# Performance work log

Measured on AMD Instinct MI355X. Metric: run time of the kernel, lower is better.

Reference implementation:

```python
import jax, jax.numpy as jnp
import numpy as np

N = 50000
D = 128
E = 800000
L = 3


def setup_inputs() -> dict:
    key = jax.random.key(0)
    ks = jax.random.split(key, 6)
    z = jax.random.normal(ks[0], (N, D), dtype=jnp.float32)
    edge_index = jax.random.randint(ks[1], (2, E), 0, N, dtype=jnp.int64)
    s1 = 1.0 / np.sqrt(2 * D)
    s2 = 1.0 / np.sqrt(D)
    # per-layer MLP params, stacked over layers: y = x @ W + b (W stored input-major)
    W1 = jax.random.uniform(ks[2], (L, 2 * D, D), jnp.float32, -s1, s1)
    b1 = jax.random.uniform(ks[3], (L, D), jnp.float32, -s1, s1)
    W2 = jax.random.uniform(ks[4], (L, D, D), jnp.float32, -s2, s2)
    b2 = jax.random.uniform(ks[5], (L, D), jnp.float32, -s2, s2)
    return {"z": z, "edge_index": edge_index, "W1": W1, "b1": b1, "W2": W2, "b2": b2}


def _edgeconv(h, src, dst, W1, b1, W2, b2):
    # message: mlp(cat[x_i, x_j]) per edge; x_i = target (dst), x_j = source (src)
    tmp = jnp.concatenate([h[dst], h[src]], axis=1)           # [E, 2D]
    m = jax.nn.relu(tmp @ W1 + b1) @ W2 + b2                  # [E, D]
    agg = jax.ops.segment_max(m, dst, num_segments=N)          # [N, D], -inf for empty
    return jnp.where(jnp.isfinite(agg), agg, 0.0)


def reference(z, edge_index, W1, b1, W2, b2):
    src = edge_index[0]
    dst = edge_index[1]
    h = z
    for l in range(L - 1):
        h = jax.nn.relu(_edgeconv(h, src, dst, W1[l], b1[l], W2[l], b2[l]))
    h = _edgeconv(h, src, dst, W1[L - 1], b1[L - 1], W2[L - 1], b2[L - 1])
    return h
```

## Files before the change

kernel.cpp:

```cpp
#include <hip/hip_runtime.h>

#define DH 128
#define NLAYER 3
typedef unsigned short ushort_t;
typedef __attribute__((ext_vector_type(8))) short bf16x8;
typedef __attribute__((ext_vector_type(4))) float f32x4;

__device__ __forceinline__ ushort_t f2bf(float a) {
    unsigned u = __float_as_uint(a);
    return (ushort_t)((u + 0x7fffu + ((u >> 16) & 1u)) >> 16);
}
__device__ __forceinline__ float bf2f(ushort_t h) {
    return __uint_as_float(((unsigned)h) << 16);
}
__device__ __forceinline__ unsigned cvtpk(float a, float b) {
    unsigned r;
    asm("v_cvt_pk_bf16_f32 %0, %1, %2" : "=v"(r) : "v"(a), "v"(b));
    return r;
}

__device__ __forceinline__ unsigned enc_f(float f) {
    unsigned u = __float_as_uint(f);
    return (u & 0x80000000u) ? ~u : (u | 0x80000000u);
}
__device__ __forceinline__ float dec_f(unsigned u) {
    unsigned b = (u & 0x80000000u) ? (u ^ 0x80000000u) : ~u;
    return __uint_as_float(b);
}
#define ENC_NEG_INF 0x007FFFFFu

__global__ void fill_u(unsigned* __restrict__ p, int n, unsigned v) {
    int i = blockIdx.x * blockDim.x + threadIdx.x;
    int stride = gridDim.x * blockDim.x;
    for (; i < n; i += stride) p[i] = v;
}

__global__ void hist_kernel(const int* __restrict__ dst, unsigned* __restrict__ cnt, int E) {
    int e = blockIdx.x * blockDim.x + threadIdx.x;
    int stride = gridDim.x * blockDim.x;
    for (; e < E; e += stride) atomicAdd(&cnt[dst[e]], 1u);
}

__global__ __launch_bounds__(1024) void scan_local(const unsigned* __restrict__ cnt,
                                                   unsigned* __restrict__ off,
                                                   unsigned* __restrict__ bsum, int n) {
    __shared__ unsigned s[1024];
    const int t = threadIdx.x;
    int idx = blockIdx.x * 1024 + t;
    unsigned v = (idx < n) ? cnt[idx] : 0u;
    s[t] = v;
    __syncthreads();
    for (int d = 1; d < 1024; d <<= 1) {
        unsigned u = (t >= d) ? s[t - d] : 0u;
        __syncthreads();
        s[t] += u;
        __syncthreads();
    }
    if (idx < n) off[idx] = s[t] - v;
    if (t == 1023) bsum[blockIdx.x] = s[t];
}
__global__ void scan_base(unsigned* __restrict__ bsum, int nb) {
    __shared__ unsigned s[64];
    const int t = threadIdx.x;
    unsigned v = (t < nb) ? bsum[t] : 0u;
    s[t] = v;
    __syncthreads();
    for (int d = 1; d < 64; d <<= 1) {
        unsigned u = (t >= d) ? s[t - d] : 0u;
        __syncthreads();
        s[t] += u;
        __syncthreads();
    }
    if (t < nb) bsum[t] = s[t] - v;
}
__global__ void scan_add(unsigned* __restrict__ off, const unsigned* __restrict__ bsum,
                         unsigned* __restrict__ cnt, int n) {
    int i = blockIdx.x * blockDim.x + threadIdx.x;
    int stride = gridDim.x * blockDim.x;
    for (; i < n; i += stride) { off[i] += bsum[i >> 10]; cnt[i] = 0u; }
}

__global__ void scatter_kernel(const int* __restrict__ src, const int* __restrict__ dst,
                               const unsigned* __restrict__ off, unsigned* __restrict__ cur,
                               int* __restrict__ s_src, int* __restrict__ s_dst, int E) {
    int e = blockIdx.x * blockDim.x + threadIdx.x;
    int stride = gridDim.x * blockDim.x;
    for (; e < E; e += stride) {
        int d = dst[e];
        unsigned p = off[d] + atomicAdd(&cur[d], 1u);
        s_src[p] = src[e];
        s_dst[p] = d;
    }
}

__global__ void convert_w(const float* __restrict__ W1, const float* __restrict__ W2,
                          ushort_t* __restrict__ W1t_hi, ushort_t* __restrict__ W1t_lo,
                          ushort_t* __restrict__ W2t_hi, ushort_t* __restrict__ W2t_lo) {
    const int T1 = NLAYER * 256 * DH, T2 = NLAYER * DH * DH;
    int i = blockIdx.x * blockDim.x + threadIdx.x;
    int stride = gridDim.x * blockDim.x;
    for (; i < T1 + T2; i += stride) {
        if (i < T1) {
            int l = i >> 15, r = i & 32767, c = r >> 7, k = r & 127;
            float w = W1[(size_t)l * 32768 + (size_t)((c < 128) ? k : 128 + k) * DH + (c & 127)];
            ushort_t hi = f2bf(w);
            W1t_hi[i] = hi; W1t_lo[i] = f2bf(w - bf2f(hi));
        } else {
            int j = i - T1;
            int l = j >> 14, r = j & 16383, c = r >> 7, k = r & 127;
            float w = W2[(size_t)l * 16384 + (size_t)k * DH + c];
            ushort_t hi = f2bf(w);
            W2t_hi[j] = hi; W2t_lo[j] = f2bf(w - bf2f(hi));
        }
    }
}

__global__ void convert_h(const float* __restrict__ z, unsigned* __restrict__ hpk, int n) {
    int i = blockIdx.x * blockDim.x + threadIdx.x;
    int stride = gridDim.x * blockDim.x;
    for (; i < n; i += stride) {
        float a = z[i];
        ushort_t hi = f2bf(a);
        ushort_t lo = f2bf(a - bf2f(hi));
        hpk[i] = (unsigned)hi | ((unsigned)lo << 16);
    }
}

__global__ __launch_bounds__(256, 2) void node_gemm(
    const unsigned* __restrict__ hpk,
    const ushort_t* __restrict__ wthi, const ushort_t* __restrict__ wtlo,
    const float* __restrict__ bias, float* __restrict__ outA, float* __restrict__ outB,
    int N, int nrb) {
    __shared__ char smem[65536];
    char* Whi = smem;
    char* Wlo = smem + 32768;
    const int bb = blockIdx.x;
    const int half = (bb >= nrb) ? 1 : 0;
    const ushort_t* whi = wthi + (half ? (size_t)128 * DH : 0);
    const ushort_t* wlo = wtlo + (half ? (size_t)128 * DH : 0);
    float* outp = half ? outB : outA;
    const int t = threadIdx.x;
    const int w = t >> 6, l = t & 63;
    for (int cid = t; cid < 2048; cid += 256) {
        int c = cid >> 4, ch = cid & 15;
        uint4 vh = *(const uint4*)(whi + (size_t)cid * 8);
        uint4 vl = *(const uint4*)(wlo + (size_t)cid * 8);
        *(uint4*)(Whi + c * 256 + ((ch ^ (c & 15)) << 4)) = vh;
        *(uint4*)(Wlo + c * 256 + ((ch ^ (c & 15)) << 4)) = vl;
    }
    const int n0 = (bb - half * nrb) * 128;
    bf16x8 ahi[2][4], alo[2][4];
    #pragma unroll
    for (int rt = 0; rt < 2; ++rt) {
        int row = n0 + w * 32 + rt * 16 + (l & 15);
        if (row >= N) row = N - 1;
        const unsigned* ph = hpk + (size_t)row * DH + 8 * (l >> 4);
        #pragma unroll
        for (int ks = 0; ks < 4; ++ks) {
            uint4 p0 = *(const uint4*)(ph + ks * 32);
            uint4 p1 = *(const uint4*)(ph + ks * 32 + 4);
            bf16x8 hv, lv;
            hv[0] = (short)(p0.x & 0xffffu); lv[0] = (short)(p0.x >> 16);
            hv[1] = (short)(p0.y & 0xffffu); lv[1] = (short)(p0.y >> 16);
            hv[2] = (short)(p0.z & 0xffffu); lv[2] = (short)(p0.z >> 16);
            hv[3] = (short)(p0.w & 0xffffu); lv[3] = (short)(p0.w >> 16);
            hv[4] = (short)(p1.x & 0xffffu); lv[4] = (short)(p1.x >> 16);
            hv[5] = (short)(p1.y & 0xffffu); lv[5] = (short)(p1.y >> 16);
            hv[6] = (short)(p1.z & 0xffffu); lv[6] = (short)(p1.z >> 16);
            hv[7] = (short)(p1.w & 0xffffu); lv[7] = (short)(p1.w >> 16);
            ahi[rt][ks] = hv; alo[rt][ks] = lv;
        }
    }
    f32x4 acc[2][8];
    #pragma unroll
    for (int rt = 0; rt < 2; ++rt)
        #pragma unroll
        for (int ct = 0; ct < 8; ++ct) acc[rt][ct] = (f32x4){0.f, 0.f, 0.f, 0.f};
    __syncthreads();
    #pragma unroll
    for (int ct = 0; ct < 8; ++ct) {
        int colv = ct * 16 + (l & 15);
        #pragma unroll
        for (int ks = 0; ks < 4; ++ks) {
            int chb = ks * 4 + (l >> 4);
            int addr = colv * 256 + ((chb ^ (colv & 15)) << 4);
            bf16x8 bh = *(const bf16x8*)(Whi + addr);
            bf16x8 bl = *(const bf16x8*)(Wlo + addr);
            #pragma unroll
            for (int rt = 0; rt < 2; ++rt) {
                acc[rt][ct] = __builtin_amdgcn_mfma_f32_16x16x32_bf16(ahi[rt][ks], bh, acc[rt][ct], 0, 0, 0);
                acc[rt][ct] = __builtin_amdgcn_mfma_f32_16x16x32_bf16(ahi[rt][ks], bl, acc[rt][ct], 0, 0, 0);
                acc[rt][ct] = __builtin_amdgcn_mfma_f32_16x16x32_bf16(alo[rt][ks], bh, acc[rt][ct], 0, 0, 0);
            }
        }
    }
    #pragma unroll
    for (int ct = 0; ct < 8; ++ct) {
        int col = ct * 16 + (l & 15);
        float bv = half ? 0.0f : bias[col];
        #pragma unroll
        for (int rt = 0; rt < 2; ++rt)
            #pragma unroll
            for (int i = 0; i < 4; ++i) {
                int row = n0 + w * 32 + rt * 16 + (l >> 4) * 4 + i;
                if (row < N) outp[(size_t)row * DH + col] = acc[rt][ct][i] + bv;
            }
    }
}

__global__ __launch_bounds__(256, 2) void edge_mlp(
    const float* __restrict__ Afp, const float* __restrict__ Bfp,
    const int* __restrict__ src, const int* __restrict__ dst,
    const ushort_t* __restrict__ w2hi, const ushort_t* __restrict__ w2lo,
    unsigned* __restrict__ agg, int E) {
    __shared__ char smem[33280];
    int* sdst = (int*)(smem + 32768);
    float* R = (float*)smem;
    const int t = threadIdx.x;
    const int w = t >> 6, l = t & 63;
    const int e0 = blockIdx.x * 128;

    if (t < 128) sdst[t] = dst[e0 + t];
    #pragma unroll
    for (int i = 0; i < 4; ++i) {
        int cid = i * 256 + t;
        int cc = cid >> 4, ch = cid & 15;
        int sc = ch ^ (cc & 15);
        uint4 vh = *(const uint4*)(w2hi + (size_t)cc * DH + sc * 8);
        uint4 vl = *(const uint4*)(w2lo + (size_t)cc * DH + sc * 8);
        *(uint4*)(smem + cid * 16) = vh;
        *(uint4*)(smem + 16384 + cid * 16) = vl;
    }

    bf16x8 ahi[2][4], alo[2][4];
    #pragma unroll
    for (int rt = 0; rt < 2; ++rt) {
        int er = w * 32 + rt * 16 + (l & 15);
        int dn = dst[e0 + er], sn = src[e0 + er];
        const float* pa = Afp + (size_t)dn * DH + 8 * (l >> 4);
        const float* pb = Bfp + (size_t)sn * DH + 8 * (l >> 4);
        #pragma unroll
        for (int ks = 0; ks < 4; ++ks) {
            float4 a0 = *(const float4*)(pa + ks * 32);
            float4 a1 = *(const float4*)(pa + ks * 32 + 4);
            float4 b0 = *(const float4*)(pb + ks * 32);
            float4 b1 = *(const float4*)(pb + ks * 32 + 4);
            float v0 = fmaxf(a0.x + b0.x, 0.f), v1 = fmaxf(a0.y + b0.y, 0.f);
            float v2 = fmaxf(a0.z + b0.z, 0.f), v3 = fmaxf(a0.w + b0.w, 0.f);
            float v4 = fmaxf(a1.x + b1.x, 0.f), v5 = fmaxf(a1.y + b1.y, 0.f);
            float v6 = fmaxf(a1.z + b1.z, 0.f), v7 = fmaxf(a1.w + b1.w, 0.f);
            unsigned h01 = cvtpk(v0, v1), h23 = cvtpk(v2, v3);
            unsigned h45 = cvtpk(v4, v5), h67 = cvtpk(v6, v7);
            float l0 = v0 - __uint_as_float(h01 << 16);
            float l1 = v1 - __uint_as_float(h01 & 0xffff0000u);
            float l2 = v2 - __uint_as_float(h23 << 16);
            float l3 = v3 - __uint_as_float(h23 & 0xffff0000u);
            float l4 = v4 - __uint_as_float(h45 << 16);
            float l5 = v5 - __uint_as_float(h45 & 0xffff0000u);
            float l6 = v6 - __uint_as_float(h67 << 16);
            float l7 = v7 - __uint_as_float(h67 & 0xffff0000u);
            unsigned q01 = cvtpk(l0, l1), q23 = cvtpk(l2, l3);
            unsigned q45 = cvtpk(l4, l5), q67 = cvtpk(l6, l7);
            uint4 hp = {h01, h23, h45, h67};
            uint4 lp = {q01, q23, q45, q67};
            ahi[rt][ks] = *(bf16x8*)&hp;
            alo[rt][ks] = *(bf16x8*)&lp;
        }
    }
    f32x4 acc[2][8];
    #pragma unroll
    for (int rt = 0; rt < 2; ++rt)
        #pragma unroll
        for (int ct = 0; ct < 8; ++ct) acc[rt][ct] = (f32x4){0.f, 0.f, 0.f, 0.f};
    __syncthreads();
    #pragma unroll
    for (int ct = 0; ct < 4; ++ct) {
        int colv = ct * 16 + (l & 15);
        #pragma unroll
        for (int ks = 0; ks < 4; ++ks) {
            int chb = ks * 4 + (l >> 4);
            int addr = colv * 256 + ((chb ^ (colv & 15)) << 4);
            bf16x8 bh = *(const bf16x8*)(smem + addr);
            bf16x8 bl = *(const bf16x8*)(smem + 16384 + addr);
            #pragma unroll
            for (int rt = 0; rt < 2; ++rt) {
                acc[rt][ct] = __builtin_amdgcn_mfma_f32_16x16x32_bf16(ahi[rt][ks], bh, acc[rt][ct], 0, 0, 0);
                acc[rt][ct] = __builtin_amdgcn_mfma_f32_16x16x32_bf16(ahi[rt][ks], bl, acc[rt][ct], 0, 0, 0);
                acc[rt][ct] = __builtin_amdgcn_mfma_f32_16x16x32_bf16(alo[rt][ks], bh, acc[rt][ct], 0, 0, 0);
            }
        }
    }
    __syncthreads();
    #pragma unroll
    for (int i = 0; i < 4; ++i) {
        int cid = i * 256 + t;
        int cc = cid >> 4, ch = cid & 15;
        int sc = ch ^ (cc & 15);
        uint4 vh = *(const uint4*)(w2hi + (size_t)(64 + cc) * DH + sc * 8);
        uint4 vl = *(const uint4*)(w2lo + (size_t)(64 + cc) * DH + sc * 8);
        *(uint4*)(smem + cid * 16) = vh;
        *(uint4*)(smem + 16384 + cid * 16) = vl;
    }
    __syncthreads();
    #pragma unroll
    for (int ct = 4; ct < 8; ++ct) {
        int colv = ct * 16 + (l & 15);
        #pragma unroll
        for (int ks = 0; ks < 4; ++ks) {
            int chb = ks * 4 + (l >> 4);
            int addr = (colv & 63) * 256 + ((chb ^ (colv & 15)) << 4);
            bf16x8 bh = *(const bf16x8*)(smem + addr);
            bf16x8 bl = *(const bf16x8*)(smem + 16384 + addr);
            #pragma unroll
            for (int rt = 0; rt < 2; ++rt) {
                acc[rt][ct] = __builtin_amdgcn_mfma_f32_16x16x32_bf16(ahi[rt][ks], bh, acc[rt][ct], 0, 0, 0);
                acc[rt][ct] = __builtin_amdgcn_mfma_f32_16x16x32_bf16(ahi[rt][ks], bl, acc[rt][ct], 0, 0, 0);
                acc[rt][ct] = __builtin_amdgcn_mfma_f32_16x16x32_bf16(alo[rt][ks], bh, acc[rt][ct], 0, 0, 0);
            }
        }
    }
    #pragma unroll
    for (int chh = 0; chh < 2; ++chh) {
        __syncthreads();
        #pragma unroll
        for (int rt = 0; rt < 2; ++rt)
            #pragma unroll
            for (int c4 = 0; c4 < 4; ++c4) {
                int ct = chh * 4 + c4;
                int col64 = c4 * 16 + (l & 15);
                #pragma unroll
                for (int i = 0; i < 4; ++i) {
                    int row = w * 32 + rt * 16 + (l >> 4) * 4 + i;
                    R[row * 64 + (col64 ^ (((row >> 2) & 3) << 4))] = acc[rt][ct][i];
                }
            }
        __syncthreads();
        const int col = l;
        const int r0 = w * 32;
        float run = R[r0 * 64 + (col ^ (((r0 >> 2) & 3) << 4))];
        int cur = sdst[r0];
        #pragma unroll
        for (int rr = r0 + 1; rr < r0 + 32; ++rr) {
            float x = R[rr * 64 + (col ^ (((rr >> 2) & 3) << 4))];
            int dd = sdst[rr];
            if (dd != cur) {
                atomicMax(&agg[(size_t)cur * DH + chh * 64 + col], enc_f(run));
                cur = dd; run = x;
            } else {
                run = fmaxf(run, x);
            }
        }
        atomicMax(&agg[(size_t)cur * DH + chh * 64 + col], enc_f(run));
    }
}

__global__ void finalize_kernel(unsigned* agg, const float* __restrict__ b2,
                                unsigned* hpk, float* __restrict__ outf, int n, int mode) {
    int i = blockIdx.x * blockDim.x + threadIdx.x;
    int stride = gridDim.x * blockDim.x;
    for (; i < n; i += stride) {
        unsigned uv = agg[i];
        float f = (uv == ENC_NEG_INF) ? 0.0f : dec_f(uv) + b2[i & (DH - 1)];
        if (mode == 0) {
            f = fmaxf(f, 0.0f);
            ushort_t hi = f2bf(f);
            ushort_t lo = f2bf(f - bf2f(hi));
            hpk[i] = (unsigned)hi | ((unsigned)lo << 16);
        } else {
            outf[i] = f;
        }
    }
}

extern "C" void kernel_launch(void* const* d_in, const int* in_sizes, int n_in,
                              void* d_out, int out_size, void* d_ws, size_t ws_size,
                              hipStream_t stream) {
    const float* z  = (const float*)d_in[0];
    const int*   ei = (const int*)d_in[1];
    const float* W1 = (const float*)d_in[2];
    const float* b1 = (const float*)d_in[3];
    const float* W2 = (const float*)d_in[4];
    const float* b2 = (const float*)d_in[5];
    const int N = 50000, D = DH, E = 800000;
    const int* srcp = ei;
    const int* dstp = ei + E;

    float* Abuf = (float*)d_ws;
    float* Bbuf = Abuf + (size_t)N * D;
    unsigned* agg = (unsigned*)(Bbuf + (size_t)N * D);
    ushort_t* W1t_hi = (ushort_t*)(agg + (size_t)N * D);
    ushort_t* W1t_lo = W1t_hi + NLAYER * 256 * D;
    ushort_t* W2t_hi = W1t_lo + NLAYER * 256 * D;
    ushort_t* W2t_lo = W2t_hi + NLAYER * D * D;
    unsigned* cnt = (unsigned*)(W2t_lo + NLAYER * D * D);
    unsigned* off = cnt + N;
    unsigned* bsum = off + N;
    int* s_src = (int*)(bsum + 64);
    int* s_dst = s_src + E;
    float* outp = (float*)d_out;

    convert_w<<<128, 256, 0, stream>>>(W1, W2, W1t_hi, W1t_lo, W2t_hi, W2t_lo);
    convert_h<<<1024, 256, 0, stream>>>(z, agg, N * D);

    const int NB = (N + 1023) / 1024;
    fill_u<<<256, 256, 0, stream>>>(cnt, N, 0u);
    hist_kernel<<<1024, 256, 0, stream>>>(dstp, cnt, E);
    scan_local<<<NB, 1024, 0, stream>>>(cnt, off, bsum, N);
    scan_base<<<1, 64, 0, stream>>>(bsum, NB);
    scan_add<<<256, 256, 0, stream>>>(off, bsum, cnt, N);
    scatter_kernel<<<1024, 256, 0, stream>>>(srcp, dstp, off, cnt, s_src, s_dst, E);

    const int nrb = (N + 127) / 128;
    for (int l = 0; l < NLAYER; ++l) {
        node_gemm<<<2 * nrb, 256, 0, stream>>>(agg,
                                               W1t_hi + ((size_t)l * 256) * D,
                                               W1t_lo + ((size_t)l * 256) * D,
                                               b1 + (size_t)l * D, Abuf, Bbuf, N, nrb);
        fill_u<<<2048, 256, 0, stream>>>(agg, N * D, ENC_NEG_INF);
        edge_mlp<<<E / 128, 256, 0, stream>>>(Abuf, Bbuf, s_src, s_dst,
                                              W2t_hi + (size_t)l * D * D,
                                              W2t_lo + (size_t)l * D * D, agg, E);
        finalize_kernel<<<2048, 256, 0, stream>>>(agg, b2 + (size_t)l * D,
                                                  agg, outp, N * D,
                                                  (l < NLAYER - 1) ? 0 : 1);
    }
}
```

Before: 782.3 us.

## Fuse input conversion and finalize into node GEMM, halve weight LDS footprint

The standalone z conversion kernel and the per-layer finalize pass are removed. node_gemm now reads fp32 z or the encoded max-aggregation buffer directly, applies bias, ReLU and empty-segment handling, then splits into bf16 hi/lo in registers. The kernel also stages the weights in two 64-column halves, cutting LDS from 64 KB to about 33 KB, which could raise occupancy but adds an extra sync and reload phase. This drops two full N×D memory passes per layer in exchange for more ALU work inside the GEMM.

```diff
diff --git a/kernel.cpp b/kernel.cpp
--- a/kernel.cpp
+++ b/kernel.cpp
@@ -115,60 +115,81 @@
     }
 }
 
-__global__ void convert_h(const float* __restrict__ z, unsigned* __restrict__ hpk, int n) {
-    int i = blockIdx.x * blockDim.x + threadIdx.x;
-    int stride = gridDim.x * blockDim.x;
-    for (; i < n; i += stride) {
-        float a = z[i];
-        ushort_t hi = f2bf(a);
-        ushort_t lo = f2bf(a - bf2f(hi));
-        hpk[i] = (unsigned)hi | ((unsigned)lo << 16);
-    }
-}
-
 __global__ __launch_bounds__(256, 2) void node_gemm(
-    const unsigned* __restrict__ hpk,
+    const float* __restrict__ zin, const unsigned* __restrict__ aggin,
+    const float* __restrict__ b2prev,
     const ushort_t* __restrict__ wthi, const ushort_t* __restrict__ wtlo,
-    const float* __restrict__ bias, float* __restrict__ outA, float* __restrict__ outB,
-    int N, int nrb) {
-    __shared__ char smem[65536];
-    char* Whi = smem;
-    char* Wlo = smem + 32768;
+    const float* __restrict__ b1, float* __restrict__ outA, float* __restrict__ outB,
+    int N, int nrb, int mode) {
+    __shared__ char smem[33280];
+    float* b2s = (float*)(smem + 32768);
+    const int t = threadIdx.x;
+    const int w = t >> 6, l = t & 63;
     const int bb = blockIdx.x;
     const int half = (bb >= nrb) ? 1 : 0;
-    const ushort_t* whi = wthi + (half ? (size_t)128 * DH : 0);
-    const ushort_t* wlo = wtlo + (half ? (size_t)128 * DH : 0);
+    const ushort_t* whi = wthi + (size_t)(half ? 128 : 0) * DH;
+    const ushort_t* wlo = wtlo + (size_t)(half ? 128 : 0) * DH;
     float* outp = half ? outB : outA;
-    const int t = threadIdx.x;
-    const int w = t >> 6, l = t & 63;
-    for (int cid = t; cid < 2048; cid += 256) {
-        int c = cid >> 4, ch = cid & 15;
-        uint4 vh = *(const uint4*)(whi + (size_t)cid * 8);
-        uint4 vl = *(const uint4*)(wlo + (size_t)cid * 8);
-        *(uint4*)(Whi + c * 256 + ((ch ^ (c & 15)) << 4)) = vh;
-        *(uint4*)(Wlo + c * 256 + ((ch ^ (c & 15)) << 4)) = vl;
-    }
     const int n0 = (bb - half * nrb) * 128;
+
+    if (t < 128) b2s[t] = mode ? b2prev[t] : 0.0f;
+    #pragma unroll
+    for (int i = 0; i < 4; ++i) {
+        int cid = i * 256 + t;
+        int cc = cid >> 4, ch = cid & 15;
+        int sc = ch ^ (cc & 15);
+        uint4 vh = *(const uint4*)(whi + (size_t)cc * DH + sc * 8);
+        uint4 vl = *(const uint4*)(wlo + (size_t)cc * DH + sc * 8);
+        *(uint4*)(smem + cid * 16) = vh;
+        *(uint4*)(smem + 16384 + cid * 16) = vl;
+    }
+    __syncthreads();
+
     bf16x8 ahi[2][4], alo[2][4];
     #pragma unroll
     for (int rt = 0; rt < 2; ++rt) {
         int row = n0 + w * 32 + rt * 16 + (l & 15);
         if (row >= N) row = N - 1;
-        const unsigned* ph = hpk + (size_t)row * DH + 8 * (l >> 4);
-        #pragma unroll
-        for (int ks = 0; ks < 4; ++ks) {
-            uint4 p0 = *(const uint4*)(ph + ks * 32);
-            uint4 p1 = *(const uint4*)(ph + ks * 32 + 4);
-            bf16x8 hv, lv;
-            hv[0] = (short)(p0.x & 0xffffu); lv[0] = (short)(p0.x >> 16);
-            hv[1] = (short)(p0.y & 0xffffu); lv[1] = (short)(p0.y >> 16);
-            hv[2] = (short)(p0.z & 0xffffu); lv[2] = (short)(p0.z >> 16);
-            hv[3] = (short)(p0.w & 0xffffu); lv[3] = (short)(p0.w >> 16);
-            hv[4] = (short)(p1.x & 0xffffu); lv[4] = (short)(p1.x >> 16);
-            hv[5] = (short)(p1.y & 0xffffu); lv[5] = (short)(p1.y >> 16);
-            hv[6] = (short)(p1.z & 0xffffu); lv[6] = (short)(p1.z >> 16);
-            hv[7] = (short)(p1.w & 0xffffu); lv[7] = (short)(p1.w >> 16);
-            ahi[rt][ks] = hv; alo[rt][ks] = lv;
+        size_t base = (size_t)row * DH + 8 * (l >> 4);
+        const int kbase = 8 * (l >> 4);
+        #pragma unroll
+        for (int ks = 0; ks < 4; ++ks) {
+            float v0, v1, v2, v3, v4, v5, v6, v7;
+            if (mode == 0) {
+                float4 a0 = *(const float4*)(zin + base + ks * 32);
+                float4 a1 = *(const float4*)(zin + base + ks * 32 + 4);
+                v0 = a0.x; v1 = a0.y; v2 = a0.z; v3 = a0.w;
+                v4 = a1.x; v5 = a1.y; v6 = a1.z; v7 = a1.w;
+            } else {
+                uint4 u0 = *(const uint4*)(aggin + base + ks * 32);
+                uint4 u1 = *(const uint4*)(aggin + base + ks * 32 + 4);
+                float4 c0 = *(const float4*)&b2s[kbase + ks * 32];
+                float4 c1 = *(const float4*)&b2s[kbase + ks * 32 + 4];
+                v0 = fmaxf((u0.x == ENC_NEG_INF) ? 0.0f : dec_f(u0.x) + c0.x, 0.0f);
+                v1 = fmaxf((u0.y == ENC_NEG_INF) ? 0.0f : dec_f(u0.y) + c0.y, 0.0f);
+                v2 = fmaxf((u0.z == ENC_NEG_INF) ? 0.0f : dec_f(u0.z) + c0.z, 0.0f);
+                v3 = fmaxf((u0.w == ENC_NEG_INF) ? 0.0f : dec_f(u0.w) + c0.w, 0.0f);
+                v4 = fmaxf((u1.x == ENC_NEG_INF) ? 0.0f : dec_f(u1.x) + c1.x, 0.0f);
+                v5 = fmaxf((u1.y == ENC_NEG_INF) ? 0.0f : dec_f(u1.y) + c1.y, 0.0f);
+                v6 = fmaxf((u1.z == ENC_NEG_INF) ? 0.0f : dec_f(u1.z) + c1.z, 0.0f);
+                v7 = fmaxf((u1.w == ENC_NEG_INF) ? 0.0f : dec_f(u1.w) + c1.w, 0.0f);
+            }
+            unsigned h01 = cvtpk(v0, v1), h23 = cvtpk(v2, v3);
+            unsigned h45 = cvtpk(v4, v5), h67 = cvtpk(v6, v7);
+            float l0 = v0 - __uint_as_float(h01 << 16);
+            float l1 = v1 - __uint_as_float(h01 & 0xffff0000u);
+            float l2 = v2 - __uint_as_float(h23 << 16);
+            float l3 = v3 - __uint_as_float(h23 & 0xffff0000u);
+            float l4 = v4 - __uint_as_float(h45 << 16);
+            float l5 = v5 - __uint_as_float(h45 & 0xffff0000u);
+            float l6 = v6 - __uint_as_float(h67 << 16);
+            float l7 = v7 - __uint_as_float(h67 & 0xffff0000u);
+            unsigned q01 = cvtpk(l0, l1), q23 = cvtpk(l2, l3);
+            unsigned q45 = cvtpk(l4, l5), q67 = cvtpk(l6, l7);
+            uint4 hp = {h01, h23, h45, h67};
+            uint4 lp = {q01, q23, q45, q67};
+            ahi[rt][ks] = *(bf16x8*)&hp;
+            alo[rt][ks] = *(bf16x8*)&lp;
         }
     }
     f32x4 acc[2][8];
@@ -176,16 +197,15 @@
     for (int rt = 0; rt < 2; ++rt)
         #pragma unroll
         for (int ct = 0; ct < 8; ++ct) acc[rt][ct] = (f32x4){0.f, 0.f, 0.f, 0.f};
-    __syncthreads();
-    #pragma unroll
-    for (int ct = 0; ct < 8; ++ct) {
+    #pragma unroll
+    for (int ct = 0; ct < 4; ++ct) {
         int colv = ct * 16 + (l & 15);
         #pragma unroll
         for (int ks = 0; ks < 4; ++ks) {
             int chb = ks * 4 + (l >> 4);
             int addr = colv * 256 + ((chb ^ (colv & 15)) << 4);
-            bf16x8 bh = *(const bf16x8*)(Whi + addr);
-            bf16x8 bl = *(const bf16x8*)(Wlo + addr);
+            bf16x8 bh = *(const bf16x8*)(smem + addr);
+            bf16x8 bl = *(const bf16x8*)(smem + 16384 + addr);
             #pragma unroll
             for (int rt = 0; rt < 2; ++rt) {
                 acc[rt][ct] = __builtin_amdgcn_mfma_f32_16x16x32_bf16(ahi[rt][ks], bh, acc[rt][ct], 0, 0, 0);
@@ -194,10 +214,39 @@
             }
         }
     }
+    __syncthreads();
+    #pragma unroll
+    for (int i = 0; i < 4; ++i) {
+        int cid = i * 256 + t;
+        int cc = cid >> 4, ch = cid & 15;
+        int sc = ch ^ (cc & 15);
+        uint4 vh = *(const uint4*)(whi + (size_t)(64 + cc) * DH + sc * 8);
+        uint4 vl = *(const uint4*)(wlo + (size_t)(64 + cc) * DH + sc * 8);
+        *(uint4*)(smem + cid * 16) = vh;
+        *(uint4*)(smem + 16384 + cid * 16) = vl;
+    }
+    __syncthreads();
+    #pragma unroll
+    for (int ct = 4; ct < 8; ++ct) {
+        int colv = ct * 16 + (l & 15);
+        #pragma unroll
+        for (int ks = 0; ks < 4; ++ks) {
+            int chb = ks * 4 + (l >> 4);
+            int addr = (colv & 63) * 256 + ((chb ^ (colv & 15)) << 4);
+            bf16x8 bh = *(const bf16x8*)(smem + addr);
+            bf16x8 bl = *(const bf16x8*)(smem + 16384 + addr);
+            #pragma unroll
+            for (int rt = 0; rt < 2; ++rt) {
+                acc[rt][ct] = __builtin_amdgcn_mfma_f32_16x16x32_bf16(ahi[rt][ks], bh, acc[rt][ct], 0, 0, 0);
+                acc[rt][ct] = __builtin_amdgcn_mfma_f32_16x16x32_bf16(ahi[rt][ks], bl, acc[rt][ct], 0, 0, 0);
+                acc[rt][ct] = __builtin_amdgcn_mfma_f32_16x16x32_bf16(alo[rt][ks], bh, acc[rt][ct], 0, 0, 0);
+            }
+        }
+    }
     #pragma unroll
     for (int ct = 0; ct < 8; ++ct) {
         int col = ct * 16 + (l & 15);
-        float bv = half ? 0.0f : bias[col];
+        float bv = half ? 0.0f : b1[col];
         #pragma unroll
         for (int rt = 0; rt < 2; ++rt)
             #pragma unroll
@@ -354,21 +403,13 @@
     }
 }
 
-__global__ void finalize_kernel(unsigned* agg, const float* __restrict__ b2,
-                                unsigned* hpk, float* __restrict__ outf, int n, int mode) {
+__global__ void finalize_kernel(const unsigned* __restrict__ agg, const float* __restrict__ b2,
+                                float* __restrict__ outf, int n) {
     int i = blockIdx.x * blockDim.x + threadIdx.x;
     int stride = gridDim.x * blockDim.x;
     for (; i < n; i += stride) {
         unsigned uv = agg[i];
-        float f = (uv == ENC_NEG_INF) ? 0.0f : dec_f(uv) + b2[i & (DH - 1)];
-        if (mode == 0) {
-            f = fmaxf(f, 0.0f);
-            ushort_t hi = f2bf(f);
-            ushort_t lo = f2bf(f - bf2f(hi));
-            hpk[i] = (unsigned)hi | ((unsigned)lo << 16);
-        } else {
-            outf[i] = f;
-        }
+        outf[i] = (uv == ENC_NEG_INF) ? 0.0f : dec_f(uv) + b2[i & (DH - 1)];
     }
 }
 
@@ -400,7 +441,6 @@
     float* outp = (float*)d_out;
 
     convert_w<<<128, 256, 0, stream>>>(W1, W2, W1t_hi, W1t_lo, W2t_hi, W2t_lo);
-    convert_h<<<1024, 256, 0, stream>>>(z, agg, N * D);
 
     const int NB = (N + 1023) / 1024;
     fill_u<<<256, 256, 0, stream>>>(cnt, N, 0u);
@@ -412,16 +452,16 @@
 
     const int nrb = (N + 127) / 128;
     for (int l = 0; l < NLAYER; ++l) {
-        node_gemm<<<2 * nrb, 256, 0, stream>>>(agg,
+        node_gemm<<<2 * nrb, 256, 0, stream>>>(z, agg,
+                                               (l > 0) ? (b2 + (size_t)(l - 1) * D) : nullptr,
                                                W1t_hi + ((size_t)l * 256) * D,
                                                W1t_lo + ((size_t)l * 256) * D,
-                                               b1 + (size_t)l * D, Abuf, Bbuf, N, nrb);
+                                               b1 + (size_t)l * D, Abuf, Bbuf,
+                                               N, nrb, (l > 0) ? 1 : 0);
         fill_u<<<2048, 256, 0, stream>>>(agg, N * D, ENC_NEG_INF);
         edge_mlp<<<E / 128, 256, 0, stream>>>(Abuf, Bbuf, s_src, s_dst,
                                               W2t_hi + (size_t)l * D * D,
                                               W2t_lo + (size_t)l * D * D, agg, E);
-        finalize_kernel<<<2048, 256, 0, stream>>>(agg, b2 + (size_t)l * D,
-                                                  agg, outp, N * D,
-                                                  (l < NLAYER - 1) ? 0 : 1);
-    }
-}
+    }
+    finalize_kernel<<<2048, 256, 0, stream>>>(agg, b2 + (size_t)2 * D, outp, N * D);
+}
```

Measured after the change: 753.2 us. -3.7%, faster.
